# Performance work log

Measured on AMD Instinct MI355X. Metric: run time of the kernel, lower is better.

The kernel has to match this reference:

```python
import jax, jax.numpy as jnp
import numpy as np

H = 12       # heads
D = 768      # hidden size
DH = D // H  # head dim = 64
SCALE = 1.0 / jnp.sqrt(jnp.float32(DH))
LN_EPS = 1e-3  # keras LayerNormalization default epsilon


def setup_inputs() -> dict:
    key = jax.random.key(0)
    ks = jax.random.split(key, 8)
    B, L = 16, 512
    s = 0.02  # truncated-normal-ish init scale
    return {
        "x": jax.random.normal(ks[0], (B, L, D), jnp.float32),
        "mask": jnp.ones((B, L), jnp.int32),
        "Wq": jax.random.normal(ks[1], (D, D), jnp.float32) * s,
        "bq": jnp.zeros((D,), jnp.float32),
        "Wk": jax.random.normal(ks[2], (D, D), jnp.float32) * s,
        "bk": jnp.zeros((D,), jnp.float32),
        "Wv": jax.random.normal(ks[3], (D, D), jnp.float32) * s,
        "bv": jnp.zeros((D,), jnp.float32),
        "Wo": jax.random.normal(ks[4], (D, D), jnp.float32) * s,
        "bo": jnp.zeros((D,), jnp.float32),
        "gamma": jnp.ones((D,), jnp.float32),
        "beta": jnp.zeros((D,), jnp.float32),
    }


def reference(x, mask, Wq, bq, Wk, bk, Wv, bv, Wo, bo, gamma, beta):
    B, L, _ = x.shape
    # QKV projections, split into heads: [B, L, H, DH]
    q = (x @ Wq + bq).reshape(B, L, H, DH)
    k = (x @ Wk + bk).reshape(B, L, H, DH)
    v = (x @ Wv + bv).reshape(B, L, H, DH)
    # scaled dot-product scores: [B, H, Lq, Lk]
    scores = jnp.einsum('bqhd,bkhd->bhqk', q, k) * SCALE
    # key-side padding mask (mask==0 -> -inf)
    neg = jnp.float32(-1e9)
    scores = jnp.where(mask[:, None, None, :] > 0, scores, neg)
    p = jax.nn.softmax(scores, axis=-1)
    # dropout rate fixed to 0.0 -> identity
    ctx = jnp.einsum('bhqk,bkhd->bqhd', p, v).reshape(B, L, D)
    attn_out = ctx @ Wo + bo
    # residual + LayerNorm (keras default eps=1e-3)
    y = x + attn_out
    mu = jnp.mean(y, axis=-1, keepdims=True)
    var = jnp.mean(jnp.square(y - mu), axis=-1, keepdims=True)
    return gamma * (y - mu) * jax.lax.rsqrt(var + LN_EPS) + beta
```

## Files before the change

### kernel.cpp

```cpp
#include <hip/hip_runtime.h>
#include <math.h>

#define NH 12
#define DMODEL 768
#define DHEAD 64
#define BATCH 16
#define SEQ 512
#define NTOK (BATCH*SEQ)
#define ATTN_SCALE 0.125f
#define LN_EPS 1e-3f
#define PADP 72
#define KITERS (DMODEL/64)

typedef __attribute__((ext_vector_type(8))) short  bf16x8;
typedef __attribute__((ext_vector_type(8))) unsigned short ushort8;
typedef __attribute__((ext_vector_type(4))) float  f32x4;

__device__ __forceinline__ unsigned short f2bf(float f) {
    unsigned int u = __float_as_uint(f);
    unsigned int r = (u + 0x7fffu + ((u >> 16) & 1u)) >> 16;
    return (unsigned short)r;
}

__device__ __forceinline__ void async_copy16(const void* g, void* l) {
    __builtin_amdgcn_global_load_lds((const __attribute__((address_space(1))) void*)g,
                                     (__attribute__((address_space(3))) void*)l,
                                     16, 0, 0);
}

__global__ __launch_bounds__(256) void prep_kernel(
    const float* __restrict__ x,
    const float* __restrict__ Wq, const float* __restrict__ Wk,
    const float* __restrict__ Wv, const float* __restrict__ Wo,
    unsigned short* __restrict__ xb,
    unsigned short* __restrict__ tq, unsigned short* __restrict__ tk,
    unsigned short* __restrict__ tv, unsigned short* __restrict__ to_)
{
    __shared__ float tile[32][33];
    const int bid = blockIdx.x;
    const int tid = threadIdx.x;

    if (bid < 6144) {
        int i = (bid * 256 + tid) * 4;
        const float4 v = *(const float4*)(x + i);
        unsigned long long pack =
              (unsigned long long)f2bf(v.x)
            | ((unsigned long long)f2bf(v.y) << 16)
            | ((unsigned long long)f2bf(v.z) << 32)
            | ((unsigned long long)f2bf(v.w) << 48);
        *(unsigned long long*)(xb + i) = pack;
        return;
    }

    const int t   = bid - 6144;
    const int zz  = t / 576;
    const int rem = t % 576;
    const float* W = (zz == 0) ? Wq : (zz == 1) ? Wk : (zz == 2) ? Wv : Wo;
    unsigned short* T = (zz == 0) ? tq : (zz == 1) ? tk : (zz == 2) ? tv : to_;

    const int bx = (rem / 24) * 32;
    const int by = (rem % 24) * 32;
    const int tx = tid & 31, ty = tid >> 5;

    #pragma unroll
    for (int i = 0; i < 32; i += 8)
        tile[ty + i][tx] = W[(size_t)(bx + ty + i) * DMODEL + by + tx];
    __syncthreads();
    #pragma unroll
    for (int i = 0; i < 32; i += 8)
        T[(size_t)(by + ty + i) * DMODEL + bx + tx] = f2bf(tile[tx][ty + i]);
}

__global__ __launch_bounds__(256, 4) void mfma_gemm_qkv(
    const unsigned short* __restrict__ xb,
    const unsigned short* __restrict__ wt0, const unsigned short* __restrict__ wt1,
    const unsigned short* __restrict__ wt2,
    const float* __restrict__ b0, const float* __restrict__ b1, const float* __restrict__ b2,
    unsigned short* __restrict__ o0, unsigned short* __restrict__ o1,
    unsigned short* __restrict__ o2)
{
    __shared__ __align__(16) unsigned short As[128 * 64];
    __shared__ __align__(16) unsigned short Bs[128 * 64];

    const int zz = blockIdx.z;
    const unsigned short* Wt = (zz == 0) ? wt0 : (zz == 1) ? wt1 : wt2;
    const float* bias        = (zz == 0) ? b0  : (zz == 1) ? b1  : b2;
    unsigned short* out      = (zz == 0) ? o0  : (zz == 1) ? o1  : o2;
    const float sc           = (zz == 0) ? ATTN_SCALE : 1.0f;

    const int tid  = threadIdx.x;
    const int lane = tid & 63;
    const int w    = tid >> 6;
    const int wm   = w >> 1, wn = w & 1;
    const int m0   = blockIdx.x * 128;
    const int n0   = blockIdx.y * 128;
    const int quad = lane >> 4;
    const int l16  = lane & 15;

    const int rloc = lane >> 3;
    const int csw  = (lane & 7) ^ rloc;
    int rowS[4];
    #pragma unroll
    for (int ii = 0; ii < 4; ++ii) rowS[ii] = (4 * w + ii) * 8 + rloc;

    const int p0 = ((quad ^ (l16 & 7)) * 8);

    f32x4 acc[4][4] = {};

    for (int kb = 0; kb < KITERS; ++kb) {
        const int k0 = kb * 64;
        #pragma unroll
        for (int ii = 0; ii < 4; ++ii) {
            async_copy16(xb + (size_t)(m0 + rowS[ii]) * DMODEL + k0 + csw * 8,
                         As + (4 * w + ii) * 512);
            async_copy16(Wt + (size_t)(n0 + rowS[ii]) * DMODEL + k0 + csw * 8,
                         Bs + (4 * w + ii) * 512);
        }
        __syncthreads();

        #pragma unroll
        for (int ks = 0; ks < 2; ++ks) {
            const int po = p0 ^ (ks * 32);
            bf16x8 a[4], b[4];
            #pragma unroll
            for (int mi = 0; mi < 4; ++mi)
                a[mi] = *(const bf16x8*)&As[(wm * 64 + mi * 16 + l16) * 64 + po];
            #pragma unroll
            for (int ni = 0; ni < 4; ++ni)
                b[ni] = *(const bf16x8*)&Bs[(wn * 64 + ni * 16 + l16) * 64 + po];
            #pragma unroll
            for (int mi = 0; mi < 4; ++mi)
                #pragma unroll
                for (int ni = 0; ni < 4; ++ni)
                    acc[mi][ni] = __builtin_amdgcn_mfma_f32_16x16x32_bf16(a[mi], b[ni], acc[mi][ni], 0, 0, 0);
        }
        __syncthreads();
    }

    if (zz == 2) {
        #pragma unroll
        for (int ni = 0; ni < 4; ++ni) {
            const int ncol = n0 + wn * 64 + ni * 16 + l16;
            const int h = ncol >> 6, dh = ncol & 63;
            const float bv = bias[ncol];
            #pragma unroll
            for (int mi = 0; mi < 4; ++mi) {
                const int mbase = m0 + wm * 64 + mi * 16 + quad * 4;
                const int bi = mbase >> 9, l = mbase & 511;
                unsigned long long pack = 0;
                #pragma unroll
                for (int r = 0; r < 4; ++r)
                    pack |= (unsigned long long)f2bf(acc[mi][ni][r] + bv) << (16 * r);
                *(unsigned long long*)(out + ((size_t)((bi * NH + h) * DHEAD + dh)) * SEQ + l) = pack;
            }
        }
    } else {
        #pragma unroll
        for (int ni = 0; ni < 4; ++ni) {
            const int ncol = n0 + wn * 64 + ni * 16 + l16;
            const int h = ncol >> 6, dh = ncol & 63;
            const float bv = bias[ncol];
            #pragma unroll
            for (int mi = 0; mi < 4; ++mi) {
                const int mbase = m0 + wm * 64 + mi * 16 + quad * 4;
                #pragma unroll
                for (int r = 0; r < 4; ++r) {
                    const int t = mbase + r;
                    const int bi = t >> 9, l = t & 511;
                    out[(size_t)((bi * NH + h) * SEQ + l) * DHEAD + dh] = f2bf((acc[mi][ni][r] + bv) * sc);
                }
            }
        }
    }
}

__global__ __launch_bounds__(256, 4) void mfma_gemm_oproj(
    const unsigned short* __restrict__ ctxb, const unsigned short* __restrict__ wto,
    const float* __restrict__ bo, const float* __restrict__ x,
    float* __restrict__ y)
{
    __shared__ __align__(16) unsigned short As[128 * 64];
    __shared__ __align__(16) unsigned short Bs[128 * 64];

    const int tid  = threadIdx.x;
    const int lane = tid & 63;
    const int w    = tid >> 6;
    const int wm   = w >> 1, wn = w & 1;
    const int m0   = blockIdx.x * 128;
    const int n0   = blockIdx.y * 128;
    const int quad = lane >> 4;
    const int l16  = lane & 15;

    const int rloc = lane >> 3;
    const int csw  = (lane & 7) ^ rloc;
    int rowS[4];
    #pragma unroll
    for (int ii = 0; ii < 4; ++ii) rowS[ii] = (4 * w + ii) * 8 + rloc;
    const int p0 = ((quad ^ (l16 & 7)) * 8);

    f32x4 acc[4][4] = {};

    for (int kb = 0; kb < KITERS; ++kb) {
        const int k0 = kb * 64;
        #pragma unroll
        for (int ii = 0; ii < 4; ++ii) {
            async_copy16(ctxb + (size_t)(m0 + rowS[ii]) * DMODEL + k0 + csw * 8,
                         As + (4 * w + ii) * 512);
            async_copy16(wto  + (size_t)(n0 + rowS[ii]) * DMODEL + k0 + csw * 8,
                         Bs + (4 * w + ii) * 512);
        }
        __syncthreads();

        #pragma unroll
        for (int ks = 0; ks < 2; ++ks) {
            const int po = p0 ^ (ks * 32);
            bf16x8 a[4], b[4];
            #pragma unroll
            for (int mi = 0; mi < 4; ++mi)
                a[mi] = *(const bf16x8*)&As[(wm * 64 + mi * 16 + l16) * 64 + po];
            #pragma unroll
            for (int ni = 0; ni < 4; ++ni)
                b[ni] = *(const bf16x8*)&Bs[(wn * 64 + ni * 16 + l16) * 64 + po];
            #pragma unroll
            for (int mi = 0; mi < 4; ++mi)
                #pragma unroll
                for (int ni = 0; ni < 4; ++ni)
                    acc[mi][ni] = __builtin_amdgcn_mfma_f32_16x16x32_bf16(a[mi], b[ni], acc[mi][ni], 0, 0, 0);
        }
        __syncthreads();
    }

    #pragma unroll
    for (int ni = 0; ni < 4; ++ni) {
        const int ncol = n0 + wn * 64 + ni * 16 + l16;
        const float bv = bo[ncol];
        #pragma unroll
        for (int mi = 0; mi < 4; ++mi) {
            const int mbase = m0 + wm * 64 + mi * 16 + quad * 4;
            #pragma unroll
            for (int r = 0; r < 4; ++r) {
                const size_t idx = (size_t)(mbase + r) * DMODEL + ncol;
                y[idx] = acc[mi][ni][r] + bv + x[idx];
            }
        }
    }
}

__global__ __launch_bounds__(256) void attn_mfma_kernel(
    const unsigned short* __restrict__ q, const unsigned short* __restrict__ k,
    const unsigned short* __restrict__ vt, const int* __restrict__ mask,
    unsigned short* __restrict__ ctxb)
{
    __shared__ __align__(16) unsigned short Qs[64 * 64];
    __shared__ __align__(16) unsigned short Ks[2][64 * 64];
    __shared__ __align__(16) unsigned short Vs[2][64 * 64];
    __shared__ __align__(16) unsigned short Ps[64 * PADP];
    __shared__ float maskV[SEQ];
    __shared__ int   cleanS[8];

    const int tid  = threadIdx.x;
    const int lane = tid & 63;
    const int w    = tid >> 6;
    const int quad = lane >> 4;
    const int l16  = lane & 15;

    const int id = blockIdx.x;
    const int qt = id / (BATCH * NH);
    const int g  = id % (BATCH * NH);
    const int b  = g / NH, h = g % NH;
    const int q0 = qt * 64;

    const unsigned short* qp  = q  + ((size_t)(b * NH + h) * SEQ + q0) * DHEAD;
    const unsigned short* kp  = k  + (size_t)(b * NH + h) * SEQ * DHEAD;
    const unsigned short* vtp = vt + (size_t)(b * NH + h) * DHEAD * SEQ;

    const int rloc = lane >> 3;
    const int csw  = (lane & 7) ^ rloc;
    const int p0   = (quad ^ (l16 & 7)) * 8;

    #pragma unroll
    for (int ii = 0; ii < 2; ++ii) {
        const int inst = 2 * w + ii;
        async_copy16(qp  + (size_t)(inst * 8 + rloc) * DHEAD + csw * 8, Qs + inst * 512);
        async_copy16(kp  + (size_t)(inst * 8 + rloc) * DHEAD + csw * 8, &Ks[0][inst * 512]);
        async_copy16(vtp + (size_t)(inst * 8 + rloc) * SEQ + csw * 8,   &Vs[0][inst * 512]);
    }
    #pragma unroll
    for (int j = 0; j < 2; ++j) {
        const int idx = tid + 256 * j;
        const bool pm = mask[b * SEQ + idx] > 0;
        maskV[idx] = pm ? 0.f : -1e9f;
        const unsigned long long bb = __ballot(pm);
        if (lane == 0) cleanS[w + 4 * j] = (bb == ~0ull) ? 1 : 0;
    }
    __syncthreads();

    bf16x8 aQ[2];
    #pragma unroll
    for (int ks = 0; ks < 2; ++ks)
        aQ[ks] = *(const bf16x8*)&Qs[(w * 16 + l16) * 64 + (p0 ^ (ks * 32))];

    bf16x8 ones;
    #pragma unroll
    for (int j = 0; j < 8; ++j) ones[j] = (short)0x3F80;

    f32x4 o[4] = {};
    f32x4 lsum = {0.f, 0.f, 0.f, 0.f};
    const f32x4 zf = {0.f, 0.f, 0.f, 0.f};

    #pragma unroll
    for (int it = 0; it < 8; ++it) {
        const int cur = it & 1;
        if (it + 1 < 8) {
            const int kt1 = (it + 1) * 64;
            #pragma unroll
            for (int ii = 0; ii < 2; ++ii) {
                const int inst = 2 * w + ii;
                async_copy16(kp  + (size_t)(kt1 + inst * 8 + rloc) * DHEAD + csw * 8,
                             &Ks[1 - cur][inst * 512]);
                async_copy16(vtp + (size_t)(inst * 8 + rloc) * SEQ + kt1 + csw * 8,
                             &Vs[1 - cur][inst * 512]);
            }
        }
        const int kt = it * 64;

        f32x4 s[4];
        #pragma unroll
        for (int ni = 0; ni < 4; ++ni) {
            bf16x8 bK0 = *(const bf16x8*)&Ks[cur][(ni * 16 + l16) * 64 + p0];
            bf16x8 bK1 = *(const bf16x8*)&Ks[cur][(ni * 16 + l16) * 64 + (p0 ^ 32)];
            f32x4 t0 = __builtin_amdgcn_mfma_f32_16x16x32_bf16(aQ[0], bK0, zf, 0, 0, 0);
            s[ni] = __builtin_amdgcn_mfma_f32_16x16x32_bf16(aQ[1], bK1, t0, 0, 0, 0);
        }
        if (cleanS[it] == 0) {
            #pragma unroll
            for (int ni = 0; ni < 4; ++ni) {
                const float mk = maskV[kt + ni * 16 + l16];
                #pragma unroll
                for (int r = 0; r < 4; ++r) s[ni][r] += mk;
            }
        }

        #pragma unroll
        for (int ni = 0; ni < 4; ++ni)
            #pragma unroll
            for (int r = 0; r < 4; ++r)
                Ps[(w * 16 + quad * 4 + r) * PADP + ni * 16 + l16]
                    = (unsigned short)(__float_as_uint(__expf(s[ni][r])) >> 16);

        bf16x8 aP[2];
        #pragma unroll
        for (int ks = 0; ks < 2; ++ks)
            aP[ks] = *(const bf16x8*)&Ps[(w * 16 + l16) * PADP + quad * 8 + ks * 32];

        lsum = __builtin_amdgcn_mfma_f32_16x16x32_bf16(aP[0], ones, lsum, 0, 0, 0);
        lsum = __builtin_amdgcn_mfma_f32_16x16x32_bf16(aP[1], ones, lsum, 0, 0, 0);

        #pragma unroll
        for (int ni = 0; ni < 4; ++ni) {
            bf16x8 bV0 = *(const bf16x8*)&Vs[cur][(ni * 16 + l16) * 64 + p0];
            bf16x8 bV1 = *(const bf16x8*)&Vs[cur][(ni * 16 + l16) * 64 + (p0 ^ 32)];
            o[ni] = __builtin_amdgcn_mfma_f32_16x16x32_bf16(aP[0], bV0, o[ni], 0, 0, 0);
            o[ni] = __builtin_amdgcn_mfma_f32_16x16x32_bf16(aP[1], bV1, o[ni], 0, 0, 0);
        }

        __syncthreads();
    }

    #pragma unroll
    for (int r = 0; r < 4; ++r) {
        const float inv = 1.f / lsum[r];
        const int tok = q0 + w * 16 + quad * 4 + r;
        #pragma unroll
        for (int ni = 0; ni < 4; ++ni)
            ctxb[(size_t)(b * SEQ + tok) * DMODEL + h * DHEAD + ni * 16 + l16]
                = f2bf(o[ni][r] * inv);
    }
}

__global__ __launch_bounds__(256) void ln_kernel(
    const float* __restrict__ y, const float* __restrict__ gamma,
    const float* __restrict__ beta, float* __restrict__ out)
{
    const int t   = blockIdx.x;
    const int tid = threadIdx.x;
    const float* row = y + (size_t)t * DMODEL;

    float vals[3];
    float s = 0.f, s2 = 0.f;
    #pragma unroll
    for (int i = 0; i < 3; ++i) {
        float vv = row[tid + 256 * i];
        vals[i] = vv;
        s  += vv;
        s2 += vv * vv;
    }
    #pragma unroll
    for (int off = 32; off > 0; off >>= 1) {
        s  += __shfl_down(s,  off);
        s2 += __shfl_down(s2, off);
    }
    __shared__ float rbuf[8];
    int w = tid >> 6;
    if ((tid & 63) == 0) { rbuf[w] = s; rbuf[4 + w] = s2; }
    __syncthreads();
    float ts  = rbuf[0] + rbuf[1] + rbuf[2] + rbuf[3];
    float ts2 = rbuf[4] + rbuf[5] + rbuf[6] + rbuf[7];
    float mu  = ts * (1.f / DMODEL);
    float var = ts2 * (1.f / DMODEL) - mu * mu;
    float inv = rsqrtf(var + LN_EPS);
    #pragma unroll
    for (int i = 0; i < 3; ++i) {
        int c = tid + 256 * i;
        out[(size_t)t * DMODEL + c] = gamma[c] * (vals[i] - mu) * inv + beta[c];
    }
}

extern "C" void kernel_launch(void* const* d_in, const int* in_sizes, int n_in,
                              void* d_out, int out_size, void* d_ws, size_t ws_size,
                              hipStream_t stream) {
    const float* x     = (const float*)d_in[0];
    const int*   mask  = (const int*)  d_in[1];
    const float* Wq    = (const float*)d_in[2];
    const float* bq    = (const float*)d_in[3];
    const float* Wk    = (const float*)d_in[4];
    const float* bk    = (const float*)d_in[5];
    const float* Wv    = (const float*)d_in[6];
    const float* bv    = (const float*)d_in[7];
    const float* Wo    = (const float*)d_in[8];
    const float* bo    = (const float*)d_in[9];
    const float* gamma = (const float*)d_in[10];
    const float* beta  = (const float*)d_in[11];
    float* out = (float*)d_out;

    const size_t perTok = (size_t)NTOK * DMODEL;
    const size_t perW   = (size_t)DMODEL * DMODEL;

    unsigned short* xb   = (unsigned short*)d_ws;
    unsigned short* wtq  = xb + perTok;
    unsigned short* wtk  = wtq + perW;
    unsigned short* wtv  = wtk + perW;
    unsigned short* wto  = wtv + perW;
    unsigned short* qb   = wto + perW;
    unsigned short* kb   = qb + perTok;
    unsigned short* vb   = kb + perTok;
    unsigned short* ctxb = vb + perTok;
    float* y = out;

    prep_kernel<<<6144 + 2304, 256, 0, stream>>>(
        x, Wq, Wk, Wv, Wo, xb, wtq, wtk, wtv, wto);

    mfma_gemm_qkv<<<dim3(NTOK / 128, DMODEL / 128, 3), 256, 0, stream>>>(
        xb, wtq, wtk, wtv, bq, bk, bv, qb, kb, vb);

    attn_mfma_kernel<<<dim3((SEQ / 64) * BATCH * NH), 256, 0, stream>>>(
        qb, kb, vb, mask, ctxb);

    mfma_gemm_oproj<<<dim3(NTOK / 128, DMODEL / 128), 256, 0, stream>>>(
        ctxb, wto, bo, x, y);

    ln_kernel<<<NTOK, 256, 0, stream>>>(y, gamma, beta, out);
}
```

Before: 200.0 us.

## Replace QKV and output GEMMs with 256x256 double-buffered ping-pong MFMA kernels

Both projection GEMMs move from 128x128 single-buffered tiles with 4 waves to 256x256 tiles with 8 waves. Each block double-buffers LDS staging with async global-to-LDS copies and interleaves MFMA groups with LDS fragment loads under explicit scheduling barriers and s_setprio. The three QKV projections become one N=2304 GEMM over the contiguous transposed weights, and block indices are remapped so neighbouring tiles land on the same XCD. The larger tiles raise data reuse and overlap loads with compute, but they need 128KB of LDS per block and leave few blocks: 288 for QKV and 96 for the output projection. That leaves many CUs idle or unevenly loaded.

```diff
diff --git a/kernel.cpp b/kernel.cpp
--- a/kernel.cpp
+++ b/kernel.cpp
@@ -10,10 +10,9 @@
 #define ATTN_SCALE 0.125f
 #define LN_EPS 1e-3f
 #define PADP 72
-#define KITERS (DMODEL/64)
+#define NKT 12
 
 typedef __attribute__((ext_vector_type(8))) short  bf16x8;
-typedef __attribute__((ext_vector_type(8))) unsigned short ushort8;
 typedef __attribute__((ext_vector_type(4))) float  f32x4;
 
 __device__ __forceinline__ unsigned short f2bf(float f) {
@@ -71,176 +70,196 @@
         T[(size_t)(by + ty + i) * DMODEL + bx + tx] = f2bf(tile[tx][ty + i]);
 }
 
-__global__ __launch_bounds__(256, 4) void mfma_gemm_qkv(
-    const unsigned short* __restrict__ xb,
-    const unsigned short* __restrict__ wt0, const unsigned short* __restrict__ wt1,
-    const unsigned short* __restrict__ wt2,
-    const float* __restrict__ b0, const float* __restrict__ b1, const float* __restrict__ b2,
+#define SBAR() do { \
+    __builtin_amdgcn_sched_barrier(0); \
+    __builtin_amdgcn_s_barrier(); \
+    __builtin_amdgcn_sched_barrier(0); \
+} while (0)
+
+#define VMWAIT0() do { \
+    __builtin_amdgcn_sched_barrier(0); \
+    asm volatile("s_waitcnt vmcnt(0)" ::: "memory"); \
+    __builtin_amdgcn_sched_barrier(0); \
+} while (0)
+
+#define STAGE8(kt, buf) do { \
+    const int _k0 = (kt) * 64; \
+    _Pragma("unroll") \
+    for (int _ii = 0; _ii < 4; ++_ii) { \
+        async_copy16(aSrc + (size_t)_ii * (8 * DMODEL) + _k0, &As[buf][(w * 4 + _ii) * 512]); \
+        async_copy16(bSrc + (size_t)_ii * (8 * DMODEL) + _k0, &Bs[buf][(w * 4 + _ii) * 512]); \
+    } } while (0)
+
+#define LDA4(dst, buf, mh) do { \
+    _Pragma("unroll") \
+    for (int _m = 0; _m < 4; ++_m) { \
+        const int _row = wm * 128 + (mh) * 64 + _m * 16 + l16; \
+        dst[_m][0] = *(const bf16x8*)&As[buf][_row * 64 + p0]; \
+        dst[_m][1] = *(const bf16x8*)&As[buf][_row * 64 + (p0 ^ 32)]; \
+    } } while (0)
+
+#define LDB2(dst, buf, nh) do { \
+    _Pragma("unroll") \
+    for (int _n = 0; _n < 2; ++_n) { \
+        const int _row = wn * 64 + (nh) * 32 + _n * 16 + l16; \
+        dst[_n][0] = *(const bf16x8*)&Bs[buf][_row * 64 + p0]; \
+        dst[_n][1] = *(const bf16x8*)&Bs[buf][_row * 64 + (p0 ^ 32)]; \
+    } } while (0)
+
+#define MM16(A, B, mh, nh) do { \
+    __builtin_amdgcn_s_setprio(1); \
+    _Pragma("unroll") \
+    for (int _k = 0; _k < 2; ++_k) \
+      _Pragma("unroll") \
+      for (int _m = 0; _m < 4; ++_m) \
+        _Pragma("unroll") \
+        for (int _n = 0; _n < 2; ++_n) \
+          acc[(mh) * 4 + _m][(nh) * 2 + _n] = __builtin_amdgcn_mfma_f32_16x16x32_bf16( \
+              A[_m][_k], B[_n][_k], acc[(mh) * 4 + _m][(nh) * 2 + _n], 0, 0, 0); \
+    __builtin_amdgcn_s_setprio(0); \
+} while (0)
+
+#define TILE4(t, c, o, hasNext) do { \
+    if (hasNext) STAGE8((t) + 1, o); \
+    LDB2(bF0, c, 0); \
+    LDB2(bF1, c, 1); \
+    MM16(aF0, bF0, 0, 0); \
+    SBAR(); \
+    LDA4(aF1, c, 1); \
+    MM16(aF0, bF1, 0, 1); \
+    SBAR(); \
+    MM16(aF1, bF1, 1, 1); \
+    SBAR(); \
+    MM16(aF1, bF0, 1, 0); \
+    if (hasNext) { VMWAIT0(); LDA4(aF0, o, 0); } \
+    SBAR(); \
+} while (0)
+
+#define GEMM8P_MAIN() \
+    f32x4 acc[8][4] = {}; \
+    bf16x8 aF0[4][2], aF1[4][2], bF0[2][2], bF1[2][2]; \
+    STAGE8(0, 0); \
+    VMWAIT0(); \
+    SBAR(); \
+    LDA4(aF0, 0, 0); \
+    _Pragma("unroll 1") \
+    for (int tt = 0; tt < NKT / 2; ++tt) { \
+        TILE4(2 * tt,     0, 1, 1); \
+        TILE4(2 * tt + 1, 1, 0, (tt < NKT / 2 - 1)); \
+    }
+
+__global__ __launch_bounds__(512, 2) void gemm8p_qkv(
+    const unsigned short* __restrict__ xb, const unsigned short* __restrict__ wt,
+    const float* __restrict__ bq, const float* __restrict__ bk, const float* __restrict__ bv,
     unsigned short* __restrict__ o0, unsigned short* __restrict__ o1,
     unsigned short* __restrict__ o2)
 {
-    __shared__ __align__(16) unsigned short As[128 * 64];
-    __shared__ __align__(16) unsigned short Bs[128 * 64];
-
-    const int zz = blockIdx.z;
-    const unsigned short* Wt = (zz == 0) ? wt0 : (zz == 1) ? wt1 : wt2;
-    const float* bias        = (zz == 0) ? b0  : (zz == 1) ? b1  : b2;
-    unsigned short* out      = (zz == 0) ? o0  : (zz == 1) ? o1  : o2;
-    const float sc           = (zz == 0) ? ATTN_SCALE : 1.0f;
+    __shared__ __align__(16) unsigned short As[2][256 * 64];
+    __shared__ __align__(16) unsigned short Bs[2][256 * 64];
+
+    const int orig = blockIdx.x;
+    const int wg   = (orig & 7) * 36 + (orig >> 3);
+    const int mt   = wg / 9, ntile = wg % 9;
+    const int m0   = mt * 256, n0 = ntile * 256;
 
     const int tid  = threadIdx.x;
     const int lane = tid & 63;
     const int w    = tid >> 6;
-    const int wm   = w >> 1, wn = w & 1;
-    const int m0   = blockIdx.x * 128;
-    const int n0   = blockIdx.y * 128;
+    const int wm   = w >> 2, wn = w & 3;
     const int quad = lane >> 4;
     const int l16  = lane & 15;
-
     const int rloc = lane >> 3;
     const int csw  = (lane & 7) ^ rloc;
-    int rowS[4];
-    #pragma unroll
-    for (int ii = 0; ii < 4; ++ii) rowS[ii] = (4 * w + ii) * 8 + rloc;
-
-    const int p0 = ((quad ^ (l16 & 7)) * 8);
-
-    f32x4 acc[4][4] = {};
-
-    for (int kb = 0; kb < KITERS; ++kb) {
-        const int k0 = kb * 64;
-        #pragma unroll
-        for (int ii = 0; ii < 4; ++ii) {
-            async_copy16(xb + (size_t)(m0 + rowS[ii]) * DMODEL + k0 + csw * 8,
-                         As + (4 * w + ii) * 512);
-            async_copy16(Wt + (size_t)(n0 + rowS[ii]) * DMODEL + k0 + csw * 8,
-                         Bs + (4 * w + ii) * 512);
-        }
-        __syncthreads();
-
-        #pragma unroll
-        for (int ks = 0; ks < 2; ++ks) {
-            const int po = p0 ^ (ks * 32);
-            bf16x8 a[4], b[4];
-            #pragma unroll
-            for (int mi = 0; mi < 4; ++mi)
-                a[mi] = *(const bf16x8*)&As[(wm * 64 + mi * 16 + l16) * 64 + po];
-            #pragma unroll
-            for (int ni = 0; ni < 4; ++ni)
-                b[ni] = *(const bf16x8*)&Bs[(wn * 64 + ni * 16 + l16) * 64 + po];
-            #pragma unroll
-            for (int mi = 0; mi < 4; ++mi)
-                #pragma unroll
-                for (int ni = 0; ni < 4; ++ni)
-                    acc[mi][ni] = __builtin_amdgcn_mfma_f32_16x16x32_bf16(a[mi], b[ni], acc[mi][ni], 0, 0, 0);
-        }
-        __syncthreads();
-    }
+    const int p0   = (quad ^ (l16 & 7)) * 8;
+
+    const unsigned short* aSrc = xb + (size_t)(m0 + w * 32 + rloc) * DMODEL + csw * 8;
+    const unsigned short* bSrc = wt + (size_t)(n0 + w * 32 + rloc) * DMODEL + csw * 8;
+
+    GEMM8P_MAIN();
+
+    const int zz    = (n0 >= 1536) ? 2 : (n0 >= 768) ? 1 : 0;
+    const int nloc0 = n0 - zz * 768;
+    const float* bias   = (zz == 0) ? bq : (zz == 1) ? bk : bv;
+    unsigned short* out = (zz == 0) ? o0 : (zz == 1) ? o1 : o2;
+    const float sc      = (zz == 0) ? ATTN_SCALE : 1.0f;
 
     if (zz == 2) {
         #pragma unroll
         for (int ni = 0; ni < 4; ++ni) {
-            const int ncol = n0 + wn * 64 + ni * 16 + l16;
-            const int h = ncol >> 6, dh = ncol & 63;
-            const float bv = bias[ncol];
-            #pragma unroll
-            for (int mi = 0; mi < 4; ++mi) {
-                const int mbase = m0 + wm * 64 + mi * 16 + quad * 4;
+            const int ncl = nloc0 + wn * 64 + ni * 16 + l16;
+            const int h = ncl >> 6, dh = ncl & 63;
+            const float bv_ = bias[ncl];
+            #pragma unroll
+            for (int mi = 0; mi < 8; ++mi) {
+                const int mbase = m0 + wm * 128 + mi * 16 + quad * 4;
                 const int bi = mbase >> 9, l = mbase & 511;
                 unsigned long long pack = 0;
                 #pragma unroll
                 for (int r = 0; r < 4; ++r)
-                    pack |= (unsigned long long)f2bf(acc[mi][ni][r] + bv) << (16 * r);
+                    pack |= (unsigned long long)f2bf(acc[mi][ni][r] + bv_) << (16 * r);
                 *(unsigned long long*)(out + ((size_t)((bi * NH + h) * DHEAD + dh)) * SEQ + l) = pack;
             }
         }
     } else {
         #pragma unroll
         for (int ni = 0; ni < 4; ++ni) {
-            const int ncol = n0 + wn * 64 + ni * 16 + l16;
-            const int h = ncol >> 6, dh = ncol & 63;
-            const float bv = bias[ncol];
-            #pragma unroll
-            for (int mi = 0; mi < 4; ++mi) {
-                const int mbase = m0 + wm * 64 + mi * 16 + quad * 4;
+            const int ncl = nloc0 + wn * 64 + ni * 16 + l16;
+            const int h = ncl >> 6, dh = ncl & 63;
+            const float bv_ = bias[ncl];
+            #pragma unroll
+            for (int mi = 0; mi < 8; ++mi) {
+                const int mbase = m0 + wm * 128 + mi * 16 + quad * 4;
                 #pragma unroll
                 for (int r = 0; r < 4; ++r) {
                     const int t = mbase + r;
                     const int bi = t >> 9, l = t & 511;
-                    out[(size_t)((bi * NH + h) * SEQ + l) * DHEAD + dh] = f2bf((acc[mi][ni][r] + bv) * sc);
+                    out[(size_t)((bi * NH + h) * SEQ + l) * DHEAD + dh] =
+                        f2bf((acc[mi][ni][r] + bv_) * sc);
                 }
             }
         }
     }
 }
 
-__global__ __launch_bounds__(256, 4) void mfma_gemm_oproj(
+__global__ __launch_bounds__(512, 2) void gemm8p_oproj(
     const unsigned short* __restrict__ ctxb, const unsigned short* __restrict__ wto,
     const float* __restrict__ bo, const float* __restrict__ x,
     float* __restrict__ y)
 {
-    __shared__ __align__(16) unsigned short As[128 * 64];
-    __shared__ __align__(16) unsigned short Bs[128 * 64];
+    __shared__ __align__(16) unsigned short As[2][256 * 64];
+    __shared__ __align__(16) unsigned short Bs[2][256 * 64];
+
+    const int orig = blockIdx.x;
+    const int wg   = (orig & 7) * 12 + (orig >> 3);
+    const int mt   = wg / 3, ntile = wg % 3;
+    const int m0   = mt * 256, n0 = ntile * 256;
 
     const int tid  = threadIdx.x;
     const int lane = tid & 63;
     const int w    = tid >> 6;
-    const int wm   = w >> 1, wn = w & 1;
-    const int m0   = blockIdx.x * 128;
-    const int n0   = blockIdx.y * 128;
+    const int wm   = w >> 2, wn = w & 3;
     const int quad = lane >> 4;
     const int l16  = lane & 15;
-
     const int rloc = lane >> 3;
     const int csw  = (lane & 7) ^ rloc;
-    int rowS[4];
-    #pragma unroll
-    for (int ii = 0; ii < 4; ++ii) rowS[ii] = (4 * w + ii) * 8 + rloc;
-    const int p0 = ((quad ^ (l16 & 7)) * 8);
-
-    f32x4 acc[4][4] = {};
-
-    for (int kb = 0; kb < KITERS; ++kb) {
-        const int k0 = kb * 64;
-        #pragma unroll
-        for (int ii = 0; ii < 4; ++ii) {
-            async_copy16(ctxb + (size_t)(m0 + rowS[ii]) * DMODEL + k0 + csw * 8,
-                         As + (4 * w + ii) * 512);
-            async_copy16(wto  + (size_t)(n0 + rowS[ii]) * DMODEL + k0 + csw * 8,
-                         Bs + (4 * w + ii) * 512);
-        }
-        __syncthreads();
-
-        #pragma unroll
-        for (int ks = 0; ks < 2; ++ks) {
-            const int po = p0 ^ (ks * 32);
-            bf16x8 a[4], b[4];
-            #pragma unroll
-            for (int mi = 0; mi < 4; ++mi)
-                a[mi] = *(const bf16x8*)&As[(wm * 64 + mi * 16 + l16) * 64 + po];
-            #pragma unroll
-            for (int ni = 0; ni < 4; ++ni)
-                b[ni] = *(const bf16x8*)&Bs[(wn * 64 + ni * 16 + l16) * 64 + po];
-            #pragma unroll
-            for (int mi = 0; mi < 4; ++mi)
-                #pragma unroll
-                for (int ni = 0; ni < 4; ++ni)
-                    acc[mi][ni] = __builtin_amdgcn_mfma_f32_16x16x32_bf16(a[mi], b[ni], acc[mi][ni], 0, 0, 0);
-        }
-        __syncthreads();
-    }
+    const int p0   = (quad ^ (l16 & 7)) * 8;
+
+    const unsigned short* aSrc = ctxb + (size_t)(m0 + w * 32 + rloc) * DMODEL + csw * 8;
+    const unsigned short* bSrc = wto  + (size_t)(n0 + w * 32 + rloc) * DMODEL + csw * 8;
+
+    GEMM8P_MAIN();
 
     #pragma unroll
     for (int ni = 0; ni < 4; ++ni) {
         const int ncol = n0 + wn * 64 + ni * 16 + l16;
-        const float bv = bo[ncol];
-        #pragma unroll
-        for (int mi = 0; mi < 4; ++mi) {
-            const int mbase = m0 + wm * 64 + mi * 16 + quad * 4;
+        const float bv_ = bo[ncol];
+        #pragma unroll
+        for (int mi = 0; mi < 8; ++mi) {
+            const int mbase = m0 + wm * 128 + mi * 16 + quad * 4;
             #pragma unroll
             for (int r = 0; r < 4; ++r) {
                 const size_t idx = (size_t)(mbase + r) * DMODEL + ncol;
-                y[idx] = acc[mi][ni][r] + bv + x[idx];
+                y[idx] = acc[mi][ni][r] + bv_ + x[idx];
             }
         }
     }
@@ -450,14 +469,12 @@
     prep_kernel<<<6144 + 2304, 256, 0, stream>>>(
         x, Wq, Wk, Wv, Wo, xb, wtq, wtk, wtv, wto);
 
-    mfma_gemm_qkv<<<dim3(NTOK / 128, DMODEL / 128, 3), 256, 0, stream>>>(
-        xb, wtq, wtk, wtv, bq, bk, bv, qb, kb, vb);
+    gemm8p_qkv<<<288, 512, 0, stream>>>(xb, wtq, bq, bk, bv, qb, kb, vb);
 
     attn_mfma_kernel<<<dim3((SEQ / 64) * BATCH * NH), 256, 0, stream>>>(
         qb, kb, vb, mask, ctxb);
 
-    mfma_gemm_oproj<<<dim3(NTOK / 128, DMODEL / 128), 256, 0, stream>>>(
-        ctxb, wto, bo, x, y);
+    gemm8p_oproj<<<96, 512, 0, stream>>>(ctxb, wto, bo, x, y);
 
     ln_kernel<<<NTOK, 256, 0, stream>>>(y, gamma, beta, out);
 }
```

Result: slower. 237.5 us (+18.8%).

## Fuse QKV GEMM into one double-buffered 256x288-tile kernel with 8 waves

Applied to the files above, without the earlier changes.

Replaces the three-way QKV GEMM (128x128 tiles, single-buffered) with one kernel. It treats the contiguous transposed Wq/Wk/Wv as a single 2304-wide weight and uses 256x288 tiles with 512 threads. Each tile's loads are double-buffered async copies into LDS, overlapped with MFMA work under raised wave priority. Blocks are remapped for locality, and the launch is exactly 256 workgroups. This costs more LDS and registers per block and depends on the weight buffers being contiguous in the workspace.

```diff
diff --git a/kernel.cpp b/kernel.cpp
--- a/kernel.cpp
+++ b/kernel.cpp
@@ -10,10 +10,9 @@
 #define ATTN_SCALE 0.125f
 #define LN_EPS 1e-3f
 #define PADP 72
-#define KITERS (DMODEL/64)
+#define NKT 12
 
 typedef __attribute__((ext_vector_type(8))) short  bf16x8;
-typedef __attribute__((ext_vector_type(8))) unsigned short ushort8;
 typedef __attribute__((ext_vector_type(4))) float  f32x4;
 
 __device__ __forceinline__ unsigned short f2bf(float f) {
@@ -71,22 +70,157 @@
         T[(size_t)(by + ty + i) * DMODEL + bx + tx] = f2bf(tile[tx][ty + i]);
 }
 
-__global__ __launch_bounds__(256, 4) void mfma_gemm_qkv(
-    const unsigned short* __restrict__ xb,
-    const unsigned short* __restrict__ wt0, const unsigned short* __restrict__ wt1,
-    const unsigned short* __restrict__ wt2,
-    const float* __restrict__ b0, const float* __restrict__ b1, const float* __restrict__ b2,
+#define SBAR() do { \
+    __builtin_amdgcn_sched_barrier(0); \
+    __builtin_amdgcn_s_barrier(); \
+    __builtin_amdgcn_sched_barrier(0); \
+} while (0)
+
+#define VMWAIT0() do { \
+    __builtin_amdgcn_sched_barrier(0); \
+    asm volatile("s_waitcnt vmcnt(0)" ::: "memory"); \
+    __builtin_amdgcn_sched_barrier(0); \
+} while (0)
+
+#define QSTAGE(kt, buf) do { \
+    const int _k0 = (kt) * 64; \
+    _Pragma("unroll") \
+    for (int _i = 0; _i < 4; ++_i) \
+        async_copy16(aSrc + (size_t)_i * (8 * DMODEL) + _k0, &As[buf][(w * 4 + _i) * 512]); \
+    _Pragma("unroll") \
+    for (int _i = 0; _i < 4; ++_i) \
+        async_copy16(bSrc + (size_t)_i * (64 * DMODEL) + _k0, &Bs[buf][(w + 8 * _i) * 512]); \
+    if (w < 4) \
+        async_copy16(bSrc + (size_t)4 * (64 * DMODEL) + _k0, &Bs[buf][(w + 32) * 512]); \
+} while (0)
+
+#define QLDA(buf) do { \
+    _Pragma("unroll") \
+    for (int _m = 0; _m < 4; ++_m) { \
+        const int _row = wm * 64 + _m * 16 + l16; \
+        aF[_m][0] = *(const bf16x8*)&As[buf][_row * 64 + p0]; \
+        aF[_m][1] = *(const bf16x8*)&As[buf][_row * 64 + (p0 ^ 32)]; \
+    } } while (0)
+
+#define QLDB(buf, nh) do { \
+    _Pragma("unroll") \
+    for (int _n = 0; _n < 3; ++_n) { \
+        const int _row = wn * 144 + ((nh) * 3 + _n) * 16 + l16; \
+        bF[_n][0] = *(const bf16x8*)&Bs[buf][_row * 64 + p0]; \
+        bF[_n][1] = *(const bf16x8*)&Bs[buf][_row * 64 + (p0 ^ 32)]; \
+    } } while (0)
+
+#define QMM(nh) do { \
+    __builtin_amdgcn_s_setprio(1); \
+    _Pragma("unroll") \
+    for (int _k = 0; _k < 2; ++_k) \
+      _Pragma("unroll") \
+      for (int _m = 0; _m < 4; ++_m) \
+        _Pragma("unroll") \
+        for (int _n = 0; _n < 3; ++_n) \
+          acc[_m][(nh) * 3 + _n] = __builtin_amdgcn_mfma_f32_16x16x32_bf16( \
+              aF[_m][_k], bF[_n][_k], acc[_m][(nh) * 3 + _n], 0, 0, 0); \
+    __builtin_amdgcn_s_setprio(0); \
+} while (0)
+
+#define QTILE(t, c, o, hasNext) do { \
+    if (hasNext) QSTAGE((t) + 1, o); \
+    QLDA(c); \
+    QLDB(c, 0); \
+    QMM(0); \
+    SBAR(); \
+    QLDB(c, 1); \
+    QMM(1); \
+    SBAR(); \
+    QLDB(c, 2); \
+    QMM(2); \
+    if (hasNext) VMWAIT0(); \
+    SBAR(); \
+} while (0)
+
+__global__ __launch_bounds__(512, 2) void gemm8p_qkv(
+    const unsigned short* __restrict__ xb, const unsigned short* __restrict__ wt,
+    const float* __restrict__ bq, const float* __restrict__ bk, const float* __restrict__ bv,
     unsigned short* __restrict__ o0, unsigned short* __restrict__ o1,
     unsigned short* __restrict__ o2)
 {
+    __shared__ __align__(16) unsigned short As[2][256 * 64];
+    __shared__ __align__(16) unsigned short Bs[2][288 * 64];
+
+    const int orig = blockIdx.x;
+    const int wg   = (orig & 7) * 32 + (orig >> 3);
+    const int m0   = (wg >> 3) * 256;
+    const int n0   = (wg & 7) * 288;
+
+    const int tid  = threadIdx.x;
+    const int lane = tid & 63;
+    const int w    = tid >> 6;
+    const int wm   = w >> 1, wn = w & 1;
+    const int quad = lane >> 4;
+    const int l16  = lane & 15;
+    const int rloc = lane >> 3;
+    const int csw  = (lane & 7) ^ rloc;
+    const int p0   = (quad ^ (l16 & 7)) * 8;
+
+    const unsigned short* aSrc = xb + (size_t)(m0 + w * 32 + rloc) * DMODEL + csw * 8;
+    const unsigned short* bSrc = wt + (size_t)(n0 + w * 8  + rloc) * DMODEL + csw * 8;
+
+    f32x4 acc[4][9] = {};
+    bf16x8 aF[4][2], bF[3][2];
+
+    QSTAGE(0, 0);
+    VMWAIT0();
+    SBAR();
+
+    #pragma unroll 1
+    for (int tt = 0; tt < NKT / 2; ++tt) {
+        QTILE(2 * tt,     0, 1, 1);
+        QTILE(2 * tt + 1, 1, 0, (tt < NKT / 2 - 1));
+    }
+
+    #pragma unroll
+    for (int nf = 0; nf < 9; ++nf) {
+        const int ncg = n0 + wn * 144 + nf * 16 + l16;
+        const int zz  = (ncg >= 1536) ? 2 : (ncg >= 768) ? 1 : 0;
+        const int ncl = ncg - zz * 768;
+        const int h = ncl >> 6, dh = ncl & 63;
+        const float bval = ((zz == 0) ? bq : (zz == 1) ? bk : bv)[ncl];
+        if (zz == 2) {
+            #pragma unroll
+            for (int mi = 0; mi < 4; ++mi) {
+                const int mbase = m0 + wm * 64 + mi * 16 + quad * 4;
+                const int bi = mbase >> 9, l = mbase & 511;
+                unsigned long long pack = 0;
+                #pragma unroll
+                for (int r = 0; r < 4; ++r)
+                    pack |= (unsigned long long)f2bf(acc[mi][nf][r] + bval) << (16 * r);
+                *(unsigned long long*)(o2 + ((size_t)((bi * NH + h) * DHEAD + dh)) * SEQ + l) = pack;
+            }
+        } else {
+            const float sc = (zz == 0) ? ATTN_SCALE : 1.0f;
+            unsigned short* out = (zz == 0) ? o0 : o1;
+            #pragma unroll
+            for (int mi = 0; mi < 4; ++mi) {
+                const int mbase = m0 + wm * 64 + mi * 16 + quad * 4;
+                #pragma unroll
+                for (int r = 0; r < 4; ++r) {
+                    const int t = mbase + r;
+                    const int bi = t >> 9, l = t & 511;
+                    out[(size_t)((bi * NH + h) * SEQ + l) * DHEAD + dh] =
+                        f2bf((acc[mi][nf][r] + bval) * sc);
+                }
+            }
+        }
+    }
+}
+
+__global__ __launch_bounds__(256, 4) void mfma_gemm_oproj(
+    const unsigned short* __restrict__ ctxb, const unsigned short* __restrict__ wto,
+    const float* __restrict__ bo, const float* __restrict__ x,
+    float* __restrict__ y)
+{
     __shared__ __align__(16) unsigned short As[128 * 64];
     __shared__ __align__(16) unsigned short Bs[128 * 64];
-
-    const int zz = blockIdx.z;
-    const unsigned short* Wt = (zz == 0) ? wt0 : (zz == 1) ? wt1 : wt2;
-    const float* bias        = (zz == 0) ? b0  : (zz == 1) ? b1  : b2;
-    unsigned short* out      = (zz == 0) ? o0  : (zz == 1) ? o1  : o2;
-    const float sc           = (zz == 0) ? ATTN_SCALE : 1.0f;
 
     const int tid  = threadIdx.x;
     const int lane = tid & 63;
@@ -102,105 +236,11 @@
     int rowS[4];
     #pragma unroll
     for (int ii = 0; ii < 4; ++ii) rowS[ii] = (4 * w + ii) * 8 + rloc;
-
     const int p0 = ((quad ^ (l16 & 7)) * 8);
 
     f32x4 acc[4][4] = {};
 
-    for (int kb = 0; kb < KITERS; ++kb) {
-        const int k0 = kb * 64;
-        #pragma unroll
-        for (int ii = 0; ii < 4; ++ii) {
-            async_copy16(xb + (size_t)(m0 + rowS[ii]) * DMODEL + k0 + csw * 8,
-                         As + (4 * w + ii) * 512);
-            async_copy16(Wt + (size_t)(n0 + rowS[ii]) * DMODEL + k0 + csw * 8,
-                         Bs + (4 * w + ii) * 512);
-        }
-        __syncthreads();
-
-        #pragma unroll
-        for (int ks = 0; ks < 2; ++ks) {
-            const int po = p0 ^ (ks * 32);
-            bf16x8 a[4], b[4];
-            #pragma unroll
-            for (int mi = 0; mi < 4; ++mi)
-                a[mi] = *(const bf16x8*)&As[(wm * 64 + mi * 16 + l16) * 64 + po];
-            #pragma unroll
-            for (int ni = 0; ni < 4; ++ni)
-                b[ni] = *(const bf16x8*)&Bs[(wn * 64 + ni * 16 + l16) * 64 + po];
-            #pragma unroll
-            for (int mi = 0; mi < 4; ++mi)
-                #pragma unroll
-                for (int ni = 0; ni < 4; ++ni)
-                    acc[mi][ni] = __builtin_amdgcn_mfma_f32_16x16x32_bf16(a[mi], b[ni], acc[mi][ni], 0, 0, 0);
-        }
-        __syncthreads();
-    }
-
-    if (zz == 2) {
-        #pragma unroll
-        for (int ni = 0; ni < 4; ++ni) {
-            const int ncol = n0 + wn * 64 + ni * 16 + l16;
-            const int h = ncol >> 6, dh = ncol & 63;
-            const float bv = bias[ncol];
-            #pragma unroll
-            for (int mi = 0; mi < 4; ++mi) {
-                const int mbase = m0 + wm * 64 + mi * 16 + quad * 4;
-                const int bi = mbase >> 9, l = mbase & 511;
-                unsigned long long pack = 0;
-                #pragma unroll
-                for (int r = 0; r < 4; ++r)
-                    pack |= (unsigned long long)f2bf(acc[mi][ni][r] + bv) << (16 * r);
-                *(unsigned long long*)(out + ((size_t)((bi * NH + h) * DHEAD + dh)) * SEQ + l) = pack;
-            }
-        }
-    } else {
-        #pragma unroll
-        for (int ni = 0; ni < 4; ++ni) {
-            const int ncol = n0 + wn * 64 + ni * 16 + l16;
-            const int h = ncol >> 6, dh = ncol & 63;
-            const float bv = bias[ncol];
-            #pragma unroll
-            for (int mi = 0; mi < 4; ++mi) {
-                const int mbase = m0 + wm * 64 + mi * 16 + quad * 4;
-                #pragma unroll
-                for (int r = 0; r < 4; ++r) {
-                    const int t = mbase + r;
-                    const int bi = t >> 9, l = t & 511;
-                    out[(size_t)((bi * NH + h) * SEQ + l) * DHEAD + dh] = f2bf((acc[mi][ni][r] + bv) * sc);
-                }
-            }
-        }
-    }
-}
-
-__global__ __launch_bounds__(256, 4) void mfma_gemm_oproj(
-    const unsigned short* __restrict__ ctxb, const unsigned short* __restrict__ wto,
-    const float* __restrict__ bo, const float* __restrict__ x,
-    float* __restrict__ y)
-{
-    __shared__ __align__(16) unsigned short As[128 * 64];
-    __shared__ __align__(16) unsigned short Bs[128 * 64];
-
-    const int tid  = threadIdx.x;
-    const int lane = tid & 63;
-    const int w    = tid >> 6;
-    const int wm   = w >> 1, wn = w & 1;
-    const int m0   = blockIdx.x * 128;
-    const int n0   = blockIdx.y * 128;
-    const int quad = lane >> 4;
-    const int l16  = lane & 15;
-
-    const int rloc = lane >> 3;
-    const int csw  = (lane & 7) ^ rloc;
-    int rowS[4];
-    #pragma unroll
-    for (int ii = 0; ii < 4; ++ii) rowS[ii] = (4 * w + ii) * 8 + rloc;
-    const int p0 = ((quad ^ (l16 & 7)) * 8);
-
-    f32x4 acc[4][4] = {};
-
-    for (int kb = 0; kb < KITERS; ++kb) {
+    for (int kb = 0; kb < NKT; ++kb) {
         const int k0 = kb * 64;
         #pragma unroll
         for (int ii = 0; ii < 4; ++ii) {
@@ -233,14 +273,14 @@
     #pragma unroll
     for (int ni = 0; ni < 4; ++ni) {
         const int ncol = n0 + wn * 64 + ni * 16 + l16;
-        const float bv = bo[ncol];
+        const float bv_ = bo[ncol];
         #pragma unroll
         for (int mi = 0; mi < 4; ++mi) {
             const int mbase = m0 + wm * 64 + mi * 16 + quad * 4;
             #pragma unroll
             for (int r = 0; r < 4; ++r) {
                 const size_t idx = (size_t)(mbase + r) * DMODEL + ncol;
-                y[idx] = acc[mi][ni][r] + bv + x[idx];
+                y[idx] = acc[mi][ni][r] + bv_ + x[idx];
             }
         }
     }
@@ -450,8 +490,7 @@
     prep_kernel<<<6144 + 2304, 256, 0, stream>>>(
         x, Wq, Wk, Wv, Wo, xb, wtq, wtk, wtv, wto);
 
-    mfma_gemm_qkv<<<dim3(NTOK / 128, DMODEL / 128, 3), 256, 0, stream>>>(
-        xb, wtq, wtk, wtv, bq, bk, bv, qb, kb, vb);
+    gemm8p_qkv<<<256, 512, 0, stream>>>(xb, wtq, bq, bk, bv, qb, kb, vb);
 
     attn_mfma_kernel<<<dim3((SEQ / 64) * BATCH * NH), 256, 0, stream>>>(
         qb, kb, vb, mask, ctxb);
```

Measured after the change: 202.3 us. About the same (+1.2%).
